# Kernel tuning notes

Measured on AMD Instinct MI355X. Metric: run time of the kernel, lower is better.

The kernel has to match this reference:

```python
import jax, jax.numpy as jnp
import numpy as np

H, W_FREQ, DIM = 16, 9, 768

def setup_inputs() -> dict:
    key = jax.random.key(0)
    k1, k2 = jax.random.split(key)
    x = jax.random.normal(k1, (256, 256, 768), dtype=jnp.float32)
    complex_weight = jax.random.normal(k2, (H, W_FREQ, DIM, 2), dtype=jnp.float32) * 0.02
    return {"x": x, "complex_weight": complex_weight}

def reference(x, complex_weight):
    B, N, C = x.shape  # N=256, C=768
    xg = x.reshape(B, 16, 16, 768)
    # 2D orthonormal rFFT over the 16x16 token grid -> (B, 16, 9, 768) complex
    xf = jnp.fft.rfftn(xg, axes=(1, 2), norm="ortho")
    weight = complex_weight[..., 0] + 1j * complex_weight[..., 1]  # (16, 9, 768)
    xf = xf * weight
    out = jnp.fft.irfftn(xf, s=(16, 16), axes=(1, 2), norm="ortho")
    return out.reshape(B, N, C)
```

## Files before the change

kernel.cpp:

```cpp
#include <hip/hip_runtime.h>


#define DIM 768
#define CT 32
#define NCT (DIM / CT)
#define TPB 8
#define IP 258

#define R2c  0.70710678118654752f
#define C1c  0.92387953251128674f
#define S1cc 0.38268343236508978f
#define INV512  (1.f / 512.f)
#define INV256  (1.f / 256.f)
#define INV1024 (1.f / 1024.f)

typedef __fp16 h2v __attribute__((ext_vector_type(2)));
union H2U { h2v h; uint32_t u; };

__device__ __forceinline__ uint32_t packh2(float a, float b) {
  H2U t; t.h = __builtin_amdgcn_cvt_pkrtz(a, b); return t.u;
}
__device__ __forceinline__ float2 unpackh2(uint32_t v) {
  H2U t; t.u = v; return make_float2((float)t.h.x, (float)t.h.y);
}

typedef __attribute__((address_space(3))) void lds_void_t;
typedef __attribute__((address_space(1))) void glb_void_t;
__device__ __forceinline__ void gload16(const float* g, const float* l) {
  __builtin_amdgcn_global_load_lds((glb_void_t*)(uintptr_t)g,
                                   (lds_void_t*)(uint32_t)(uintptr_t)l, 16, 0, 0);
}

#define BAR_LGKM() { asm volatile("s_waitcnt lgkmcnt(0)" ::: "memory"); __builtin_amdgcn_s_barrier(); }
#define BAR_ALL()  { asm volatile("s_waitcnt vmcnt(0) lgkmcnt(0)" ::: "memory"); __builtin_amdgcn_s_barrier(); }

template <int SGN>
__device__ __forceinline__ void fft16(float* xr, float* xi) {
#define SWP(a, b) { float t_ = xr[a]; xr[a] = xr[b]; xr[b] = t_; t_ = xi[a]; xi[a] = xi[b]; xi[b] = t_; }
  SWP(1, 8) SWP(2, 4) SWP(3, 12) SWP(5, 10) SWP(7, 14) SWP(11, 13)
#undef SWP
#define BF1(a, b) { float tr = xr[b], ti = xi[b]; xr[b] = xr[a] - tr; xi[b] = xi[a] - ti; xr[a] += tr; xi[a] += ti; }
#define BFI(a, b) { float tr, ti; if (SGN < 0) { tr = xi[b]; ti = -xr[b]; } else { tr = -xi[b]; ti = xr[b]; } \
                    xr[b] = xr[a] - tr; xi[b] = xi[a] - ti; xr[a] += tr; xi[a] += ti; }
#define BFW(a, b, Wr, Wi) { float tr = (Wr) * xr[b] - (Wi) * xi[b], ti = (Wr) * xi[b] + (Wi) * xr[b]; \
                            xr[b] = xr[a] - tr; xi[b] = xi[a] - ti; xr[a] += tr; xi[a] += ti; }
  BF1(0, 1) BF1(2, 3) BF1(4, 5) BF1(6, 7) BF1(8, 9) BF1(10, 11) BF1(12, 13) BF1(14, 15)
  BF1(0, 2) BF1(4, 6) BF1(8, 10) BF1(12, 14)
  BFI(1, 3) BFI(5, 7) BFI(9, 11) BFI(13, 15)
  BF1(0, 4) BF1(8, 12)
  BFW(1, 5, R2c, SGN * R2c) BFW(9, 13, R2c, SGN * R2c)
  BFI(2, 6) BFI(10, 14)
  BFW(3, 7, -R2c, SGN * R2c) BFW(11, 15, -R2c, SGN * R2c)
  BF1(0, 8)
  BFW(1, 9, C1c, SGN * S1cc)
  BFW(2, 10, R2c, SGN * R2c)
  BFW(3, 11, S1cc, SGN * C1c)
  BFI(4, 12)
  BFW(5, 13, -S1cc, SGN * C1c)
  BFW(6, 14, -R2c, SGN * R2c)
  BFW(7, 15, -C1c, SGN * S1cc)
#undef BF1
#undef BFI
#undef BFW
}

__global__ __launch_bounds__(256, 4) void gf8_kernel(const float* __restrict__ x,
                                                     const float* __restrict__ w,
                                                     float* __restrict__ out) {
  __shared__ __align__(16) uint32_t E[16 * IP];
  __shared__ __align__(16) float xs[8192];

  const int blk = blockIdx.x;
  const int ct = blk >> 5;
  const int bg = blk & 31;
  const int c0 = ct * CT;
  const int t  = threadIdx.x;
  const int wv = t >> 6;
  const int l  = t & 63;
  const int r  = t >> 4;
  const int p  = t & 15;

  const float* gsrc0 = x + c0 + (size_t)(wv * 64 + (l >> 3)) * DIM + (l & 7) * 4;
  const float* ldst0 = xs + wv * 2048;

#define PREF(bb) {                                                         \
    const float* gs_ = gsrc0 + (size_t)(bb) * 196608;                      \
    _Pragma("unroll")                                                      \
    for (int q_ = 0; q_ < 8; ++q_)                                         \
      gload16(gs_ + q_ * 8 * DIM, ldst0 + q_ * 256);                       \
  }

  PREF(bg * TPB);
  __syncthreads();

#pragma unroll 1
  for (int it = 0; it < TPB; ++it) {
    const int b = bg * TPB + it;

    {
      const float2* xp = (const float2*)xs + r * 256 + p;
      float zr[16], zi[16];
#pragma unroll
      for (int j = 0; j < 16; j++) { float2 v = xp[j * 16]; zr[j] = v.x; zi[j] = v.y; }
      fft16<-1>(zr, zi);
      {
        uint2 v; v.x = packh2(zr[0], zr[8]); v.y = packh2(zi[0], zi[8]);
        *(uint2*)&E[2 * (r * 129 + p)] = v;
      }
#pragma unroll
      for (int k = 1; k <= 7; k++) {
        const int m = 16 - k;
        float Ar = zr[k] + zr[m], Ai = zi[k] - zi[m];
        float Br = zi[k] + zi[m], Bi = zr[m] - zr[k];
        uint2 v; v.x = packh2(Ar, Ai); v.y = packh2(Br, Bi);
        *(uint2*)&E[2 * (r * 129 + k * 16 + p)] = v;
      }
    }
    BAR_LGKM();

    {
      const int s = t >> 5;
      const int c = t & 31;
      float gr[16], gi[16];
      const uint32_t* col = E + s * 32 + c;
#pragma unroll
      for (int i = 0; i < 16; i++) { float2 v = unpackh2(col[i * IP]); gr[i] = v.x; gi[i] = v.y; }
      BAR_LGKM();

      fft16<-1>(gr, gi);
      if (s == 0) {
        const float* wc = w + (size_t)(c0 + c) * 2;
        {
          float2 a0 = *(const float2*)(wc);
          float2 a8 = *(const float2*)(wc + 12288);
          float2 b0 = *(const float2*)(wc + 8 * 13824);
          float2 b8 = *(const float2*)(wc + 8 * 13824 + 12288);
          gr[0] = gr[0] * (a0.x * INV256);
          gi[0] = gi[0] * (a8.x * INV256);
          gr[8] = gr[8] * (b0.x * INV256);
          gi[8] = gi[8] * (b8.x * INV256);
        }
#pragma unroll
        for (int k = 1; k <= 7; k++) {
          const int m = 16 - k;
          float2 a0 = *(const float2*)(wc + (size_t)k * 13824);
          float2 m0 = *(const float2*)(wc + (size_t)m * 13824);
          float2 a8 = *(const float2*)(wc + (size_t)k * 13824 + 12288);
          float2 m8 = *(const float2*)(wc + (size_t)m * 13824 + 12288);
          float Vpr = (a0.x + m0.x + a8.x + m8.x) * INV1024;
          float Vpi = (a0.y - m0.y + a8.y - m8.y) * INV1024;
          float Vmr = (a0.x + m0.x - a8.x - m8.x) * INV1024;
          float Vmi = (a0.y - m0.y - a8.y + m8.y) * INV1024;
          float ur = gr[k], ui = gi[k], vr = gr[m], vi = gi[m];
          float nkr = ur * Vpr - ui * Vpi + vr * Vmr + vi * Vmi;
          float nki = ur * Vpi + ui * Vpr + vr * Vmi - vi * Vmr;
          float nmr = vr * Vpr + vi * Vpi + ur * Vmr - ui * Vmi;
          float nmi = vi * Vpr - vr * Vpi - ur * Vmi - ui * Vmr;
          gr[k] = nkr; gi[k] = nki; gr[m] = nmr; gi[m] = nmi;
        }
      } else {
        const float* wp = w + (size_t)(s * 768 + c0 + c) * 2;
#pragma unroll
        for (int k1 = 0; k1 < 16; k1++) {
          float2 wv2 = *(const float2*)(wp + (size_t)k1 * 13824);
          const float wr_ = wv2.x * INV512, wi_ = wv2.y * INV512;
          float yr = gr[k1] * wr_ - gi[k1] * wi_;
          float yi = gr[k1] * wi_ + gi[k1] * wr_;
          gr[k1] = yr; gi[k1] = yi;
        }
      }
      fft16<1>(gr, gi);

      asm volatile("" ::: "memory");
      if (it + 1 < TPB) PREF(b + 1);

      uint32_t* colo = E + s * 32 + c;
#pragma unroll
      for (int n1 = 0; n1 < 16; n1++) { colo[n1 * IP] = packh2(gr[n1], gi[n1]); }
    }
    BAR_LGKM();

    {
      float hr[16], hq[16];
#pragma unroll
      for (int k = 0; k <= 7; k++) {
        uint2 v = *(const uint2*)&E[2 * (r * 129 + k * 16 + p)];
        float2 lo = unpackh2(v.x);
        float2 hi = unpackh2(v.y);
        if (k == 0) {
          hr[0] = lo.x; hq[0] = hi.x;
          hr[8] = lo.y; hq[8] = hi.y;
        } else {
          hr[k] = lo.x - hi.y;      hq[k] = lo.y + hi.x;
          hr[16 - k] = lo.x + hi.y; hq[16 - k] = hi.x - lo.y;
        }
      }
      fft16<1>(hr, hq);
      float2* op = (float2*)(out + (size_t)b * 196608 + (size_t)r * 12288 + c0) + p;
#pragma unroll
      for (int n2 = 0; n2 < 16; n2++) { op[n2 * 384] = make_float2(hr[n2], hq[n2]); }
    }
    BAR_ALL();
  }
}

extern "C" void kernel_launch(void* const* d_in, const int* in_sizes, int n_in,
                              void* d_out, int out_size, void* d_ws, size_t ws_size,
                              hipStream_t stream) {
  const float* x = (const float*)d_in[0];
  const float* w = (const float*)d_in[1];
  float* out = (float*)d_out;
  dim3 grid(NCT * 32);
  dim3 block(256);
  hipLaunchKernelGGL(gf8_kernel, grid, block, 0, stream, x, w, out);
}
```

Baseline: 120.4 us.

## Issue next-batch prefetch earlier and relax end-of-iteration vmcnt wait

The global-to-LDS prefetch of the next batch's input tile now starts right after the first barrier instead of after the column FFT stage. This gives the loads more time to overlap with compute. The end-of-iteration barrier waits only with vmcnt(16), so the 16 output stores can stay in flight while the older prefetch loads are guaranteed complete. Weight loads are also hoisted ahead of the forward column FFT in the non-DC branch to hide their latency. The code relies on in-order vmcnt counting of loads and stores together, and hoisting the weight loads may raise register pressure.

```diff
diff --git a/kernel.cpp b/kernel.cpp
--- a/kernel.cpp
+++ b/kernel.cpp
@@ -31,8 +31,9 @@
                                    (lds_void_t*)(uint32_t)(uintptr_t)l, 16, 0, 0);
 }
 
-#define BAR_LGKM() { asm volatile("s_waitcnt lgkmcnt(0)" ::: "memory"); __builtin_amdgcn_s_barrier(); }
-#define BAR_ALL()  { asm volatile("s_waitcnt vmcnt(0) lgkmcnt(0)" ::: "memory"); __builtin_amdgcn_s_barrier(); }
+#define BARL()     { asm volatile("s_waitcnt lgkmcnt(0)" ::: "memory"); __builtin_amdgcn_s_barrier(); }
+#define BAR_PREF() { asm volatile("s_waitcnt vmcnt(16) lgkmcnt(0)" ::: "memory"); __builtin_amdgcn_s_barrier(); }
+#define BAR_VM0()  { asm volatile("s_waitcnt vmcnt(0) lgkmcnt(0)" ::: "memory"); __builtin_amdgcn_s_barrier(); }
 
 template <int SGN>
 __device__ __forceinline__ void fft16(float* xr, float* xi) {
@@ -64,10 +65,10 @@
 #undef BFW
 }
 
-__global__ __launch_bounds__(256, 4) void gf8_kernel(const float* __restrict__ x,
-                                                     const float* __restrict__ w,
-                                                     float* __restrict__ out) {
-  __shared__ __align__(16) uint32_t E[16 * IP];
+__global__ __launch_bounds__(256, 4) void gf10_kernel(const float* __restrict__ x,
+                                                      const float* __restrict__ w,
+                                                      float* __restrict__ out) {
+  __shared__ __align__(8)  uint32_t E[16 * IP];
   __shared__ __align__(16) float xs[8192];
 
   const int blk = blockIdx.x;
@@ -79,24 +80,24 @@
   const int l  = t & 63;
   const int r  = t >> 4;
   const int p  = t & 15;
-
-  const float* gsrc0 = x + c0 + (size_t)(wv * 64 + (l >> 3)) * DIM + (l & 7) * 4;
-  const float* ldst0 = xs + wv * 2048;
-
-#define PREF(bb) {                                                         \
-    const float* gs_ = gsrc0 + (size_t)(bb) * 196608;                      \
-    _Pragma("unroll")                                                      \
-    for (int q_ = 0; q_ < 8; ++q_)                                         \
-      gload16(gs_ + q_ * 8 * DIM, ldst0 + q_ * 256);                       \
+  const int s  = t >> 5;
+  const int c  = t & 31;
+
+  const float* gpf = x + (size_t)(bg * TPB) * 196608
+                       + (size_t)(wv * 64 + (l >> 3)) * DIM + c0 + (l & 7) * 4;
+  const float* lpf0 = xs + wv * 2048;
+  const float* ob   = out + (size_t)(bg * TPB) * 196608 + c0;
+
+  {
+    const float* gs_ = gpf; const float* ls_ = lpf0;
+#pragma unroll 1
+    for (int q_ = 0; q_ < 8; ++q_) { gload16(gs_, ls_); gs_ += 8 * DIM; ls_ += 256; }
+    gpf += 196608;
   }
-
-  PREF(bg * TPB);
-  __syncthreads();
+  BAR_VM0();
 
 #pragma unroll 1
   for (int it = 0; it < TPB; ++it) {
-    const int b = bg * TPB + it;
-
     {
       const float2* xp = (const float2*)xs + r * 256 + p;
       float zr[16], zi[16];
@@ -116,19 +117,24 @@
         *(uint2*)&E[2 * (r * 129 + k * 16 + p)] = v;
       }
     }
-    BAR_LGKM();
+    BARL();
+
+    if (it + 1 < TPB) {
+      const float* gs_ = gpf; const float* ls_ = lpf0;
+#pragma unroll 1
+      for (int q_ = 0; q_ < 8; ++q_) { gload16(gs_, ls_); gs_ += 8 * DIM; ls_ += 256; }
+      gpf += 196608;
+    }
 
     {
-      const int s = t >> 5;
-      const int c = t & 31;
       float gr[16], gi[16];
       const uint32_t* col = E + s * 32 + c;
 #pragma unroll
       for (int i = 0; i < 16; i++) { float2 v = unpackh2(col[i * IP]); gr[i] = v.x; gi[i] = v.y; }
-      BAR_LGKM();
-
-      fft16<-1>(gr, gi);
+      BARL();
+
       if (s == 0) {
+        fft16<-1>(gr, gi);
         const float* wc = w + (size_t)(c0 + c) * 2;
         {
           float2 a0 = *(const float2*)(wc);
@@ -158,27 +164,30 @@
           float nmi = vi * Vpr - vr * Vpi - ur * Vmi - ui * Vmr;
           gr[k] = nkr; gi[k] = nki; gr[m] = nmr; gi[m] = nmi;
         }
+        fft16<1>(gr, gi);
       } else {
+        float wvr[16], wvi[16];
         const float* wp = w + (size_t)(s * 768 + c0 + c) * 2;
 #pragma unroll
         for (int k1 = 0; k1 < 16; k1++) {
           float2 wv2 = *(const float2*)(wp + (size_t)k1 * 13824);
-          const float wr_ = wv2.x * INV512, wi_ = wv2.y * INV512;
-          float yr = gr[k1] * wr_ - gi[k1] * wi_;
-          float yi = gr[k1] * wi_ + gi[k1] * wr_;
+          wvr[k1] = wv2.x * INV512; wvi[k1] = wv2.y * INV512;
+        }
+        fft16<-1>(gr, gi);
+#pragma unroll
+        for (int k1 = 0; k1 < 16; k1++) {
+          float yr = gr[k1] * wvr[k1] - gi[k1] * wvi[k1];
+          float yi = gr[k1] * wvi[k1] + gi[k1] * wvr[k1];
           gr[k1] = yr; gi[k1] = yi;
         }
-      }
-      fft16<1>(gr, gi);
-
-      asm volatile("" ::: "memory");
-      if (it + 1 < TPB) PREF(b + 1);
+        fft16<1>(gr, gi);
+      }
 
       uint32_t* colo = E + s * 32 + c;
 #pragma unroll
       for (int n1 = 0; n1 < 16; n1++) { colo[n1 * IP] = packh2(gr[n1], gi[n1]); }
     }
-    BAR_LGKM();
+    BARL();
 
     {
       float hr[16], hq[16];
@@ -196,11 +205,12 @@
         }
       }
       fft16<1>(hr, hq);
-      float2* op = (float2*)(out + (size_t)b * 196608 + (size_t)r * 12288 + c0) + p;
+      float2* op = (float2*)(ob + (size_t)r * 12288) + p;
 #pragma unroll
       for (int n2 = 0; n2 < 16; n2++) { op[n2 * 384] = make_float2(hr[n2], hq[n2]); }
     }
-    BAR_ALL();
+    ob += 196608;
+    BAR_PREF();
   }
 }
 
@@ -212,5 +222,5 @@
   float* out = (float*)d_out;
   dim3 grid(NCT * 32);
   dim3 block(256);
-  hipLaunchKernelGGL(gf8_kernel, grid, block, 0, stream, x, w, out);
-}
+  hipLaunchKernelGGL(gf10_kernel, grid, block, 0, stream, x, w, out);
+}
```

Result: slower. 169.0 us (+40.4%).
